# Performance work log

Measured on AMD Instinct MI355X. Metric: run time of the kernel, lower is better.

Reference implementation:

```python
import jax, jax.numpy as jnp
import numpy as np
from jax import lax


def _gru(x, h, Wi, Wh, bi, bh):
    # PyTorch GRUCell: gates ordered (r, z, n)
    gi = x @ Wi + bi
    gh = h @ Wh + bh
    ir, iz, in_ = jnp.split(gi, 3, axis=-1)
    hr, hz, hn = jnp.split(gh, 3, axis=-1)
    r = jax.nn.sigmoid(ir + hr)
    z = jax.nn.sigmoid(iz + hz)
    n = jnp.tanh(in_ + r * hn)
    return (1.0 - z) * n + z * h


def _mlp(x, W1, b1, W2, b2):
    return jax.nn.leaky_relu(x @ W1 + b1, 0.1) @ W2 + b2


def setup_inputs() -> dict:
    key = jax.random.key(0)
    S, Wn, E, DH, OD = 128, 3968, 128, 512, 2  # scenarios, world agents, embed, dec hidden, out dim
    N, H = S + Wn, 4 * E
    ks = jax.random.split(key, 32)
    rn = lambda k, sh, s: (jax.random.normal(k, sh, jnp.float32) * s)
    # ragged segment ids: every scenario gets >=1 world agent, rest random
    extra = jax.random.randint(ks[0], (Wn - S,), 0, S)
    seg_ids = jnp.sort(jnp.concatenate([jnp.arange(S), extra])).astype(jnp.int32)
    sH = 1.0 / np.sqrt(H)
    return {
        'goals': rn(ks[1], (N, 2), 1.0),
        'agn_dyn': rn(ks[2], (N, E), 1.0),
        'agn_ccls': rn(ks[3], (N, E), 1.0),
        'agn_int': rn(ks[4], (N, E), 1.0),
        'seg_ids': seg_ids,
        'sdc_h0': rn(ks[5], (S, H), 1.0),
        'wld_h0': rn(ks[6], (Wn, H), 1.0),
        'gol_W': rn(ks[7], (2, E), 1.0 / np.sqrt(2.0)),
        'gol_b': rn(ks[8], (E,), 0.01),
        'sdc_Wi': rn(ks[9], (H, 3 * H), sH), 'sdc_Wh': rn(ks[10], (H, 3 * H), sH),
        'sdc_bi': rn(ks[11], (3 * H,), 0.01), 'sdc_bh': rn(ks[12], (3 * H,), 0.01),
        'wld_Wi': rn(ks[13], (H, 3 * H), sH), 'wld_Wh': rn(ks[14], (H, 3 * H), sH),
        'wld_bi': rn(ks[15], (3 * H,), 0.01), 'wld_bh': rn(ks[16], (3 * H,), 0.01),
        'sdc_o1W': rn(ks[17], (H, DH), sH), 'sdc_o1b': rn(ks[18], (DH,), 0.01),
        'sdc_o2W': rn(ks[19], (DH, OD), 1.0 / np.sqrt(DH)), 'sdc_o2b': rn(ks[20], (OD,), 0.01),
        'wld_o1W': rn(ks[21], (H, DH), sH), 'wld_o1b': rn(ks[22], (DH,), 0.01),
        'wld_o2W': rn(ks[23], (DH, OD), 1.0 / np.sqrt(DH)), 'wld_o2b': rn(ks[24], (OD,), 0.01),
    }


def reference(goals, agn_dyn, agn_ccls, agn_int, seg_ids, sdc_h0, wld_h0,
              gol_W, gol_b, sdc_Wi, sdc_Wh, sdc_bi, sdc_bh,
              wld_Wi, wld_Wh, wld_bi, wld_bh,
              sdc_o1W, sdc_o1b, sdc_o2W, sdc_o2b,
              wld_o1W, wld_o1b, wld_o2W, wld_o2b):
    S = sdc_h0.shape[0]
    agn_gol = goals @ gol_W + gol_b                                  # [N, E]
    enc = jnp.concatenate([agn_gol, agn_dyn, agn_ccls, agn_int], 1)  # [N, 4E]
    sdc_h = _gru(enc[:S], sdc_h0, sdc_Wi, sdc_Wh, sdc_bi, sdc_bh)    # step 0
    wld_h = _gru(enc[S:], wld_h0, wld_Wi, wld_Wh, wld_bi, wld_bh)

    def step(carry, _):
        sh, wh = carry
        sdc_in = jax.ops.segment_max(wh, seg_ids, num_segments=S,
                                     indices_are_sorted=True)        # per-scenario max-pool
        wld_in = sh[seg_ids]                                         # broadcast SDC to its group
        sh2 = _gru(sdc_in, sh, sdc_Wi, sdc_Wh, sdc_bi, sdc_bh)
        wh2 = _gru(wld_in, wh, wld_Wi, wld_Wh, wld_bi, wld_bh)
        return (sh2, wh2), (sh2, wh2)

    (_, _), (sdc_hs, wld_hs) = lax.scan(step, (sdc_h, wld_h), None, length=79)
    sdc_all = jnp.concatenate([sdc_h[None], sdc_hs], 0).transpose(1, 0, 2)  # [S, 80, 4E]
    wld_all = jnp.concatenate([wld_h[None], wld_hs], 0).transpose(1, 0, 2)  # [W, 80, 4E]
    out_sdc = _mlp(sdc_all, sdc_o1W, sdc_o1b, sdc_o2W, sdc_o2b)
    out_wld = _mlp(wld_all, wld_o1W, wld_o1b, wld_o2W, wld_o2b)
    return jnp.concatenate([out_sdc, out_wld], 0)                    # [N, 80, out_dim]
```

## Files before the change

### kernel.cpp

```cpp
#include <hip/hip_runtime.h>


typedef __attribute__((ext_vector_type(8))) short short8;
typedef __attribute__((ext_vector_type(4))) float f32x4;
typedef unsigned short u16;
typedef unsigned int u32;

#define DEV __device__ __forceinline__

constexpr int S  = 128;
constexpr int NR = 4096;
constexpr int H  = 512;
constexpr int TH = 1536;
constexpr int SLOT = NR * H;
constexpr int SEGSZ = S * H;

struct P {
  const float *goals, *dyn, *ccls, *inte;
  const int *seg;
  const float *sdc_h0, *wld_h0;
  const float *golW, *golb;
  const float *sdcbi, *sdcbh, *wldbi, *wldbh;
  const float *sdco1b, *sdco2W, *sdco2b;
  const float *wldo1b, *wldo2W, *wldo2b;
  const float *sdcWi, *sdcWh, *wldWi, *wldWh, *sdco1W, *wldo1W;
  float *out;
  float *whf;
  u16   *ring;
  u16   *enc;
  u16   *WT;
  u16   *o1T;
  float *G;
  u32   *segb;
  u16   *segbf;
  float *part;
  int t;
};

DEV u16 f2bf(float f) {
  u32 u = __float_as_uint(f);
  u32 r = u + 0x7FFFu + ((u >> 16) & 1u);
  return (u16)(r >> 16);
}
DEV u32 flipf(float f) {
  u32 u = __float_as_uint(f);
  return (u & 0x80000000u) ? ~u : (u | 0x80000000u);
}
DEV float unflip(u32 s) {
  u32 u = (s & 0x80000000u) ? (s & 0x7FFFFFFFu) : ~s;
  return __uint_as_float(u);
}
DEV float sigm(float x)  { return 1.0f / (1.0f + __expf(-x)); }
DEV float tanh_(float x) { return 2.0f / (1.0f + __expf(-2.0f * x)) - 1.0f; }

DEV f32x4 mfma16(short8 a, short8 b, f32x4 c) {
  return __builtin_amdgcn_mfma_f32_16x16x32_bf16(a, b, c, 0, 0, 0);
}

DEV void gload16(const void* g, void* l) {
  __builtin_amdgcn_global_load_lds(
      (const __attribute__((address_space(1))) void*)g,
      (__attribute__((address_space(3))) void*)l, 16, 0, 0);
}

DEV short8 lds_frag(const u16* lds, int row, int g) {
  return *(const short8*)(lds + row * 64 + ((g ^ (row & 7)) << 3));
}

__global__ __launch_bounds__(256) void k_prep(P p) {
  const int b = blockIdx.x, tid = threadIdx.x;
  __shared__ float ltf[64 * 65];
  if (b < 896) {
    int nt, kt, Nn; const float* src; u16* dst;
    if (b < 768) {
      int m = b / 192, t2 = b % 192;
      nt = t2 % 24; kt = t2 / 24; Nn = TH;
      src = (m == 0) ? p.sdcWi : (m == 1) ? p.sdcWh : (m == 2) ? p.wldWi : p.wldWh;
      dst = p.WT + m * TH * H;
    } else {
      int bb = b - 768, m = bb / 64, t2 = bb % 64;
      nt = t2 % 8; kt = t2 / 8; Nn = H;
      src = m ? p.wldo1W : p.sdco1W;
      dst = p.o1T + m * H * H;
    }
    for (int it = 0; it < 16; ++it) {
      int kl = it * 4 + (tid >> 6), nl = tid & 63;
      ltf[nl * 65 + kl] = src[(kt * 64 + kl) * Nn + nt * 64 + nl];
    }
    __syncthreads();
    for (int it = 0; it < 2; ++it) {
      int nl = it * 32 + (tid >> 3), k8 = (tid & 7) * 8;
      short8 v;
#pragma unroll
      for (int e = 0; e < 8; ++e) v[e] = (short)f2bf(ltf[nl * 65 + k8 + e]);
      *(short8*)(dst + (nt * 64 + nl) * H + kt * 64 + k8) = v;
    }
  } else if (b < 960) {
    int r0 = (b - 896) * 64;
    for (int i = 0; i < 128; ++i) {
      int idx = i * 256 + tid, row = r0 + (idx >> 9), c = idx & 511;
      float v;
      if (c < 128)      v = p.goals[row*2]*p.golW[c] + p.goals[row*2+1]*p.golW[128+c] + p.golb[c];
      else if (c < 256) v = p.dyn [row*128 + c - 128];
      else if (c < 384) v = p.ccls[row*128 + c - 256];
      else              v = p.inte[row*128 + c - 384];
      p.enc[row * H + c] = f2bf(v);
    }
  } else if (b < 1024) {
    int r0 = (b - 960) * 64;
    for (int i = 0; i < 128; ++i) {
      int idx = i * 256 + tid, row = r0 + (idx >> 9), c = idx & 511;
      float v = (row < S) ? p.sdc_h0[row * H + c] : p.wld_h0[(row - S) * H + c];
      p.whf[SLOT + row * H + c] = v;
      p.ring[7 * SLOT + row * H + c] = f2bf(v);
    }
  } else {
    int base = (b - 1024) * 16384;
    for (int i = 0; i < 64; ++i) p.segb[base + i * 256 + tid] = 0u;
  }
}

__global__ __launch_bounds__(256) void k_big0(P p) {
  const int b = blockIdx.x, tid = threadIdx.x;
  const int rt = b >> 3, cg = b & 7;
  const bool sdc = rt < 2;
  const int w = tid >> 6, lr = (tid >> 4) & 3, lc = tid & 15;
  __shared__ u16 sm[16384];
  const u16* WiT = p.WT + (sdc ? 0 : 2) * TH * H;
  const u16* WhT = p.WT + (sdc ? 1 : 3) * TH * H;

  f32x4 ai[3][4], ah[3][4];
  f32x4 zero = {0.f, 0.f, 0.f, 0.f};
#pragma unroll
  for (int g = 0; g < 3; ++g)
#pragma unroll
    for (int mt = 0; mt < 4; ++mt) { ai[g][mt] = zero; ah[g][mt] = zero; }

  for (int pass = 0; pass < 2; ++pass) {
    const u16* A  = pass ? (p.ring + 7 * SLOT + rt * 64 * H) : (p.enc + rt * 64 * H);
    const u16* BT = pass ? WhT : WiT;
    for (int kc = 0; kc < H; kc += 64) {
      __syncthreads();
#pragma unroll
      for (int it = 0; it < 8; ++it) {
        int u = it * 256 + tid;
        int gs = (u ^ (u >> 3)) & 7;
        const u16* src;
        if (u < 512) {
          src = A + (u >> 3) * H + kc + gs * 8;
        } else {
          int v = u - 512;
          int g = v >> 9, m = (v >> 3) & 63;
          src = BT + (g * H + cg * 64 + m) * H + kc + gs * 8;
        }
        gload16(src, sm + (it * 256 + (tid & 192)) * 8);
      }
      __syncthreads();
#pragma unroll
      for (int s2 = 0; s2 < 2; ++s2) {
        const int gk = s2 * 4 + lr;
        short8 av[4], bv[3];
#pragma unroll
        for (int mt = 0; mt < 4; ++mt) av[mt] = lds_frag(sm, mt * 16 + lc, gk);
#pragma unroll
        for (int g = 0; g < 3; ++g) bv[g] = lds_frag(sm + 4096 + g * 4096, w * 16 + lc, gk);
#pragma unroll
        for (int g = 0; g < 3; ++g)
#pragma unroll
          for (int mt = 0; mt < 4; ++mt) {
            f32x4 r = pass ? ah[g][mt] : ai[g][mt];
            r = mfma16(av[mt], bv[g], r);
            if (pass) ah[g][mt] = r; else ai[g][mt] = r;
          }
      }
    }
  }
  const float* bi = sdc ? p.sdcbi : p.wldbi;
  const float* bh = sdc ? p.sdcbh : p.wldbh;
  const int col = cg * 64 + w * 16 + lc;
  const float bir = bi[col], biz = bi[H + col], bin = bi[2 * H + col];
  const float bhr = bh[col], bhz = bh[H + col], bhn = bh[2 * H + col];
#pragma unroll
  for (int mt = 0; mt < 4; ++mt)
#pragma unroll
    for (int i = 0; i < 4; ++i) {
      int grow = rt * 64 + mt * 16 + lr * 4 + i;
      float r = sigm(ai[0][mt][i] + bir + ah[0][mt][i] + bhr);
      float z = sigm(ai[1][mt][i] + biz + ah[1][mt][i] + bhz);
      float n = tanh_(ai[2][mt][i] + bin + r * (ah[2][mt][i] + bhn));
      float h = p.whf[SLOT + grow * H + col];
      float h2 = (1.f - z) * n + z * h;
      p.whf[grow * H + col] = h2;
      p.ring[grow * H + col] = f2bf(h2);
      if (!sdc) {
        int scen = p.seg[grow - S];
        atomicMax(p.segb + scen * H + col, flipf(h2));
      }
    }
}

__global__ __launch_bounds__(512) void k_small(P p) {
  const int b = blockIdx.x, tid = threadIdx.x;
  const int gtid = b * 512 + tid;
  u32* sb = p.segb + (p.t & 1) * SEGSZ;
  if (gtid < 16384) ((uint4*)sb)[gtid] = make_uint4(0u, 0u, 0u, 0u);
  const u32* sp = p.segb + ((p.t - 1) & 1) * SEGSZ;
  if (gtid < 16384) {
    uint4 q = ((const uint4*)sp)[gtid];
    u32 lo = (u32)f2bf(unflip(q.x)) | ((u32)f2bf(unflip(q.y)) << 16);
    u32 hi = (u32)f2bf(unflip(q.z)) | ((u32)f2bf(unflip(q.w)) << 16);
    ((u32*)p.segbf)[gtid * 2]     = lo;
    ((u32*)p.segbf)[gtid * 2 + 1] = hi;
  }
  const int rh = b / 24, nc = b % 24;
  const int wv = tid >> 6, wm = wv >> 2, wn = wv & 3;
  const int lr = (tid >> 4) & 3, lc = tid & 15;
  __shared__ u16 sm[16384];
  const u16* Ab = p.ring + ((p.t - 1) & 7) * SLOT + rh * 64 * H;
  const u16* Wb = p.WT + 2 * TH * H;

  f32x4 acc[2];
  f32x4 zero = {0.f, 0.f, 0.f, 0.f};
  acc[0] = zero; acc[1] = zero;

  for (int kc = 0; kc < H; kc += 128) {
    __syncthreads();
#pragma unroll
    for (int it = 0; it < 4; ++it) {
      int u = it * 512 + tid;
      int q = u >> 9;
      int m = (u >> 3) & 63, g = u & 7;
      int gs = g ^ (m & 7);
      int ko = kc + ((q & 1) << 6) + gs * 8;
      const u16* src = (q < 2) ? (Ab + m * H + ko)
                               : (Wb + (nc * 64 + m) * H + ko);
      gload16(src, sm + (it * 512 + (tid & 448)) * 8);
    }
    __syncthreads();
#pragma unroll
    for (int c = 0; c < 2; ++c)
#pragma unroll
      for (int s2 = 0; s2 < 2; ++s2) {
        const int gk = s2 * 4 + lr;
        short8 bv = lds_frag(sm + (2 + c) * 4096, wn * 16 + lc, gk);
#pragma unroll
        for (int mt = 0; mt < 2; ++mt)
          acc[mt] = mfma16(
              lds_frag(sm + c * 4096, wm * 32 + mt * 16 + lc, gk), bv, acc[mt]);
      }
  }
  const int colb = nc * 64 + wn * 16 + lc;
  const float bi = p.wldbi[colb];
#pragma unroll
  for (int mt = 0; mt < 2; ++mt)
#pragma unroll
    for (int i = 0; i < 4; ++i)
      p.G[(rh * 64 + wm * 32 + mt * 16 + lr * 4 + i) * TH + colb] = acc[mt][i] + bi;
}

__global__ __launch_bounds__(512) void k_big(P p) {
  const int b = blockIdx.x, tid = threadIdx.x;
  const int lr = (tid >> 4) & 3, lc = tid & 15;
  __shared__ u16 sm[16384];
  const int tp = (p.t - 1) & 7, tn = p.t & 7;
  const float* whfP = p.whf + ((p.t - 1) & 1) * SLOT;
  float* whfN = p.whf + (p.t & 1) * SLOT;
  u16* ringN = p.ring + tn * SLOT;

  if (b < 496) {
    const int wv = tid >> 6, wm = wv >> 2, wn = wv & 3;
    const int rt = b >> 3, cg = b & 7;
    const u16* Abase = p.ring + tp * SLOT + (S + rt * 64) * H;
    const u16* Bbase = p.WT + 3 * TH * H;
    f32x4 acc[3][2];
    f32x4 zero = {0.f, 0.f, 0.f, 0.f};
#pragma unroll
    for (int g = 0; g < 3; ++g) { acc[g][0] = zero; acc[g][1] = zero; }

    for (int kc = 0; kc < H; kc += 64) {
      __syncthreads();
#pragma unroll
      for (int it = 0; it < 4; ++it) {
        int u = it * 512 + tid;
        int gs = (u ^ (u >> 3)) & 7;
        const u16* src;
        if (u < 512) {
          src = Abase + (u >> 3) * H + kc + gs * 8;
        } else {
          int v = u - 512;
          int g = v >> 9, m = (v >> 3) & 63;
          src = Bbase + (g * H + cg * 64 + m) * H + kc + gs * 8;
        }
        gload16(src, sm + (it * 512 + (tid & 448)) * 8);
      }
      __syncthreads();
#pragma unroll
      for (int s2 = 0; s2 < 2; ++s2) {
        const int gk = s2 * 4 + lr;
        short8 av[2], bv[3];
#pragma unroll
        for (int mt = 0; mt < 2; ++mt)
          av[mt] = lds_frag(sm, wm * 32 + mt * 16 + lc, gk);
#pragma unroll
        for (int g = 0; g < 3; ++g)
          bv[g] = lds_frag(sm + 4096 + g * 4096, wn * 16 + lc, gk);
#pragma unroll
        for (int g = 0; g < 3; ++g)
#pragma unroll
          for (int mt = 0; mt < 2; ++mt) acc[g][mt] = mfma16(av[mt], bv[g], acc[g][mt]);
      }
    }
    const int col = cg * 64 + wn * 16 + lc;
    const float bhr = p.wldbh[col], bhz = p.wldbh[H + col], bhn = p.wldbh[2 * H + col];
    u32* sb = p.segb + (p.t & 1) * SEGSZ;
    int curSc = -1; float curMx = 0.f;
#pragma unroll
    for (int mt = 0; mt < 2; ++mt)
#pragma unroll
      for (int i = 0; i < 4; ++i) {
        int wrow = rt * 64 + wm * 32 + mt * 16 + lr * 4 + i;
        int grow = S + wrow;
        int scen = p.seg[wrow];
        const float* Gr = p.G + scen * TH;
        float r = sigm(Gr[col]          + acc[0][mt][i] + bhr);
        float z = sigm(Gr[H + col]      + acc[1][mt][i] + bhz);
        float n = tanh_(Gr[2 * H + col] + r * (acc[2][mt][i] + bhn));
        float h = whfP[grow * H + col];
        float h2 = (1.f - z) * n + z * h;
        whfN[grow * H + col] = h2;
        ringN[grow * H + col] = f2bf(h2);
        if (scen == curSc) curMx = fmaxf(curMx, h2);
        else {
          if (curSc >= 0) atomicMax(sb + curSc * H + col, flipf(curMx));
          curSc = scen; curMx = h2;
        }
      }
    atomicMax(sb + curSc * H + col, flipf(curMx));
  } else {
    const int w = tid >> 6;
    if (w >= 4) return;
    const int ab = b - 496, rh = ab >> 5, cgx = ab & 31;
    f32x4 ai[3], ah[3];
    f32x4 zero = {0.f, 0.f, 0.f, 0.f};
#pragma unroll
    for (int g = 0; g < 3; ++g) { ai[g] = zero; ah[g] = zero; }

    for (int pass = 0; pass < 2; ++pass) {
      const u16* A  = pass ? (p.ring + tp * SLOT + rh * 64 * H)
                           : (p.segbf + rh * 64 * H);
      const u16* BT = p.WT + (pass ? 1 : 0) * TH * H;
      for (int kc = 0; kc < H; kc += 64) {
        __syncthreads();
#pragma unroll
        for (int it = 0; it < 4; ++it) {
          int u = it * 256 + tid;
          if (u < 896) {
            int gs = (u ^ (u >> 3)) & 7;
            const u16* src;
            if (u < 512) {
              src = A + (u >> 3) * H + kc + gs * 8;
            } else {
              int v = u - 512;
              int m = v >> 3;
              src = BT + ((m >> 4) * H + cgx * 16 + (m & 15)) * H + kc + gs * 8;
            }
            gload16(src, sm + (it * 256 + (tid & 192)) * 8);
          }
        }
        __syncthreads();
#pragma unroll
        for (int s2 = 0; s2 < 2; ++s2) {
          const int gk = s2 * 4 + lr;
          short8 a = lds_frag(sm, w * 16 + lc, gk);
#pragma unroll
          for (int g = 0; g < 3; ++g) {
            f32x4 r = pass ? ah[g] : ai[g];
            r = mfma16(a, lds_frag(sm + 4096, g * 16 + lc, gk), r);
            if (pass) ah[g] = r; else ai[g] = r;
          }
        }
      }
    }
    const int col = cgx * 16 + lc;
    const float bir = p.sdcbi[col], biz = p.sdcbi[H + col], bin = p.sdcbi[2 * H + col];
    const float bhr = p.sdcbh[col], bhz = p.sdcbh[H + col], bhn = p.sdcbh[2 * H + col];
#pragma unroll
    for (int i = 0; i < 4; ++i) {
      int srow = rh * 64 + w * 16 + lr * 4 + i;
      float r = sigm(ai[0][i] + bir + ah[0][i] + bhr);
      float z = sigm(ai[1][i] + biz + ah[1][i] + bhz);
      float n = tanh_(ai[2][i] + bin + r * (ah[2][i] + bhn));
      float h = whfP[srow * H + col];
      float h2 = (1.f - z) * n + z * h;
      whfN[srow * H + col] = h2;
      ringN[srow * H + col] = f2bf(h2);
    }
  }
}

__global__ __launch_bounds__(256) void k_mlp(P p) {
  const int b = blockIdx.x, tid = threadIdx.x;
  const int rt = b >> 2, ct = b & 3;
  const int slot = rt >> 5, rtile = rt & 31;
  const bool sdc = (rtile == 0);
  const int w = tid >> 6, lr = (tid >> 4) & 3, lc = tid & 15;
  __shared__ u16 sm[16384];
  const u16* A  = p.ring + slot * SLOT + rtile * 128 * H;
  const u16* Bb = p.o1T + (sdc ? 0 : 1) * H * H + (ct * 128) * H;
  const float* o1b = sdc ? p.sdco1b : p.wldo1b;
  const float* o2W = sdc ? p.sdco2W : p.wldo2W;

  f32x4 acc[8][2];
  f32x4 zero = {0.f, 0.f, 0.f, 0.f};
#pragma unroll
  for (int mt = 0; mt < 8; ++mt) { acc[mt][0] = zero; acc[mt][1] = zero; }

  for (int kc = 0; kc < H; kc += 64) {
    __syncthreads();
#pragma unroll
    for (int it = 0; it < 8; ++it) {
      int u = it * 256 + tid;
      int gs = (u ^ (u >> 3)) & 7;
      const u16* src;
      if (u < 1024) src = A  + (u >> 3) * H + kc + gs * 8;
      else          src = Bb + ((u >> 3) & 127) * H + kc + gs * 8;
      gload16(src, sm + (it * 256 + (tid & 192)) * 8);
    }
    __syncthreads();
#pragma unroll
    for (int s2 = 0; s2 < 2; ++s2) {
      const int gk = s2 * 4 + lr;
      short8 av[8], bv[2];
#pragma unroll
      for (int mt = 0; mt < 8; ++mt) av[mt] = lds_frag(sm, mt * 16 + lc, gk);
#pragma unroll
      for (int c2 = 0; c2 < 2; ++c2) bv[c2] = lds_frag(sm + 8192, w * 32 + c2 * 16 + lc, gk);
#pragma unroll
      for (int mt = 0; mt < 8; ++mt)
#pragma unroll
        for (int c2 = 0; c2 < 2; ++c2) acc[mt][c2] = mfma16(av[mt], bv[c2], acc[mt][c2]);
    }
  }
  __syncthreads();
  float* red = (float*)sm;
#pragma unroll
  for (int mt = 0; mt < 8; ++mt) {
    float q0[4] = {0.f, 0.f, 0.f, 0.f}, q1[4] = {0.f, 0.f, 0.f, 0.f};
#pragma unroll
    for (int c2 = 0; c2 < 2; ++c2) {
      int col = ct * 128 + w * 32 + c2 * 16 + lc;
      float b1 = o1b[col], w0 = o2W[col * 2], w1 = o2W[col * 2 + 1];
#pragma unroll
      for (int i = 0; i < 4; ++i) {
        float v = acc[mt][c2][i] + b1;
        v = v > 0.f ? v : 0.1f * v;
        q0[i] += v * w0; q1[i] += v * w1;
      }
    }
#pragma unroll
    for (int off = 1; off < 16; off <<= 1)
#pragma unroll
      for (int i = 0; i < 4; ++i) {
        q0[i] += __shfl_xor(q0[i], off);
        q1[i] += __shfl_xor(q1[i], off);
      }
    if (lc == 0)
#pragma unroll
      for (int i = 0; i < 4; ++i) {
        int row = mt * 16 + lr * 4 + i;
        red[(w * 128 + row) * 2 + 0] = q0[i];
        red[(w * 128 + row) * 2 + 1] = q1[i];
      }
  }
  __syncthreads();
  {
    int row = tid >> 1, od = tid & 1;
    float sum = red[(0 * 128 + row) * 2 + od] + red[(1 * 128 + row) * 2 + od] +
                red[(2 * 128 + row) * 2 + od] + red[(3 * 128 + row) * 2 + od];
    int r = slot * 4096 + rtile * 128 + row;
    p.part[ct * 65536 + r * 2 + od] = sum;
  }
}

__global__ __launch_bounds__(256) void k_mlp2(P p) {
  const int gtid = blockIdx.x * 256 + threadIdx.x;
  for (int i = gtid; i < 65536; i += 16384) {
    int r = i >> 1, od = i & 1;
    int row = r & 4095, slot = r >> 12;
    float v = p.part[i] + p.part[65536 + i] + p.part[131072 + i] + p.part[196608 + i];
    v += (row < S ? p.sdco2b : p.wldo2b)[od];
    p.out[row * 160 + (p.t + slot) * 2 + od] = v;
  }
}

extern "C" void kernel_launch(void* const* d_in, const int* in_sizes, int n_in,
                              void* d_out, int out_size, void* d_ws, size_t ws_size,
                              hipStream_t stream) {
  P prm;
  prm.goals  = (const float*)d_in[0];
  prm.dyn    = (const float*)d_in[1];
  prm.ccls   = (const float*)d_in[2];
  prm.inte   = (const float*)d_in[3];
  prm.seg    = (const int*)  d_in[4];
  prm.sdc_h0 = (const float*)d_in[5];
  prm.wld_h0 = (const float*)d_in[6];
  prm.golW   = (const float*)d_in[7];
  prm.golb   = (const float*)d_in[8];
  prm.sdcWi  = (const float*)d_in[9];
  prm.sdcWh  = (const float*)d_in[10];
  prm.sdcbi  = (const float*)d_in[11];
  prm.sdcbh  = (const float*)d_in[12];
  prm.wldWi  = (const float*)d_in[13];
  prm.wldWh  = (const float*)d_in[14];
  prm.wldbi  = (const float*)d_in[15];
  prm.wldbh  = (const float*)d_in[16];
  prm.sdco1W = (const float*)d_in[17];
  prm.sdco1b = (const float*)d_in[18];
  prm.sdco2W = (const float*)d_in[19];
  prm.sdco2b = (const float*)d_in[20];
  prm.wldo1W = (const float*)d_in[21];
  prm.wldo1b = (const float*)d_in[22];
  prm.wldo2W = (const float*)d_in[23];
  prm.wldo2b = (const float*)d_in[24];
  prm.out = (float*)d_out;

  char* ws = (char*)d_ws;
  prm.whf   = (float*)(ws + 0);
  prm.ring  = (u16*)  (ws + 16777216);
  prm.enc   = (u16*)  (ws + 50331648);
  prm.WT    = (u16*)  (ws + 54525952);
  prm.o1T   = (u16*)  (ws + 60817408);
  prm.G     = (float*)(ws + 61865984);
  prm.segb  = (u32*)  (ws + 62652416);
  prm.segbf = (u16*)  (ws + 50331648);
  prm.part  = (float*)(ws + 50331648 + 131072);

  prm.t = 0;
  k_prep<<<1028, 256, 0, stream>>>(prm);
  k_big0<<<512, 256, 0, stream>>>(prm);
  for (int t = 1; t < 80; ++t) {
    prm.t = t;
    k_small<<<48, 512, 0, stream>>>(prm);
    k_big<<<560, 512, 0, stream>>>(prm);
    if ((t & 7) == 7) {
      P pm = prm;
      pm.t = t - 7;
      k_mlp<<<1024, 256, 0, stream>>>(pm);
      k_mlp2<<<64, 256, 0, stream>>>(pm);
    }
  }
}
```

Measured before the change: 2.442 ms.

## Move SDC GRU step into small kernel and fuse MLP reduction into step

```diff
diff --git a/kernel.cpp b/kernel.cpp
--- a/kernel.cpp
+++ b/kernel.cpp
@@ -32,7 +32,6 @@
   u16   *o1T;
   float *G;
   u32   *segb;
-  u16   *segbf;
   float *part;
   int t;
 };
@@ -63,6 +62,22 @@
       (__attribute__((address_space(3))) void*)l, 16, 0, 0);
 }
 
+DEV void stage_bf(u16* lds, const u16* src, int stride, int rows, int tid) {
+  for (int u = tid; u < rows * 8; u += 256) {
+    int m = u >> 3, g = u & 7, gs = g ^ (m & 7);
+    *(short8*)(lds + (u << 3)) = *(const short8*)(src + m * stride + (gs << 3));
+  }
+}
+DEV void stage_seg(u16* lds, const u32* src, int stride, int tid) {
+  for (int u = tid; u < 512; u += 256) {
+    int m = u >> 3, g = u & 7, gs = g ^ (m & 7);
+    const u32* pp = src + m * stride + (gs << 3);
+    short8 v;
+#pragma unroll
+    for (int e = 0; e < 8; ++e) v[e] = (short)f2bf(unflip(pp[e]));
+    *(short8*)(lds + (u << 3)) = v;
+  }
+}
 DEV short8 lds_frag(const u16* lds, int row, int g) {
   return *(const short8*)(lds + row * 64 + ((g ^ (row & 7)) << 3));
 }
@@ -97,22 +112,34 @@
     }
   } else if (b < 960) {
     int r0 = (b - 896) * 64;
-    for (int i = 0; i < 128; ++i) {
-      int idx = i * 256 + tid, row = r0 + (idx >> 9), c = idx & 511;
-      float v;
-      if (c < 128)      v = p.goals[row*2]*p.golW[c] + p.goals[row*2+1]*p.golW[128+c] + p.golb[c];
-      else if (c < 256) v = p.dyn [row*128 + c - 128];
-      else if (c < 384) v = p.ccls[row*128 + c - 256];
-      else              v = p.inte[row*128 + c - 384];
-      p.enc[row * H + c] = f2bf(v);
+    for (int i = 0; i < 32; ++i) {
+      int idx = i * 256 + tid;
+      int row = r0 + (idx >> 7), c4 = (idx & 127) * 4;
+      float4 v;
+      if (c4 < 128) {
+        float g0 = p.goals[row * 2], g1 = p.goals[row * 2 + 1];
+        v.x = g0 * p.golW[c4]     + g1 * p.golW[128 + c4]     + p.golb[c4];
+        v.y = g0 * p.golW[c4 + 1] + g1 * p.golW[128 + c4 + 1] + p.golb[c4 + 1];
+        v.z = g0 * p.golW[c4 + 2] + g1 * p.golW[128 + c4 + 2] + p.golb[c4 + 2];
+        v.w = g0 * p.golW[c4 + 3] + g1 * p.golW[128 + c4 + 3] + p.golb[c4 + 3];
+      } else if (c4 < 256) v = *(const float4*)(p.dyn  + row * 128 + c4 - 128);
+      else if (c4 < 384)   v = *(const float4*)(p.ccls + row * 128 + c4 - 256);
+      else                 v = *(const float4*)(p.inte + row * 128 + c4 - 384);
+      ushort4 o;
+      o.x = f2bf(v.x); o.y = f2bf(v.y); o.z = f2bf(v.z); o.w = f2bf(v.w);
+      *(ushort4*)(p.enc + row * H + c4) = o;
     }
   } else if (b < 1024) {
     int r0 = (b - 960) * 64;
-    for (int i = 0; i < 128; ++i) {
-      int idx = i * 256 + tid, row = r0 + (idx >> 9), c = idx & 511;
-      float v = (row < S) ? p.sdc_h0[row * H + c] : p.wld_h0[(row - S) * H + c];
-      p.whf[SLOT + row * H + c] = v;
-      p.ring[7 * SLOT + row * H + c] = f2bf(v);
+    for (int i = 0; i < 32; ++i) {
+      int idx = i * 256 + tid;
+      int row = r0 + (idx >> 7), c4 = (idx & 127) * 4;
+      float4 v = (row < S) ? *(const float4*)(p.sdc_h0 + row * H + c4)
+                           : *(const float4*)(p.wld_h0 + (row - S) * H + c4);
+      *(float4*)(p.whf + SLOT + row * H + c4) = v;
+      ushort4 o;
+      o.x = f2bf(v.x); o.y = f2bf(v.y); o.z = f2bf(v.z); o.w = f2bf(v.w);
+      *(ushort4*)(p.ring + 7 * SLOT + row * H + c4) = o;
     }
   } else {
     int base = (b - 1024) * 16384;
@@ -120,21 +147,22 @@
   }
 }
 
-__global__ __launch_bounds__(256) void k_big0(P p) {
+__global__ __launch_bounds__(512) void k_big0(P p) {
   const int b = blockIdx.x, tid = threadIdx.x;
   const int rt = b >> 3, cg = b & 7;
   const bool sdc = rt < 2;
-  const int w = tid >> 6, lr = (tid >> 4) & 3, lc = tid & 15;
+  const int wv = tid >> 6, wm = wv >> 2, wn = wv & 3;
+  const int lr = (tid >> 4) & 3, lc = tid & 15;
   __shared__ u16 sm[16384];
   const u16* WiT = p.WT + (sdc ? 0 : 2) * TH * H;
   const u16* WhT = p.WT + (sdc ? 1 : 3) * TH * H;
 
-  f32x4 ai[3][4], ah[3][4];
+  f32x4 ai[3][2], ah[3][2];
   f32x4 zero = {0.f, 0.f, 0.f, 0.f};
 #pragma unroll
   for (int g = 0; g < 3; ++g)
 #pragma unroll
-    for (int mt = 0; mt < 4; ++mt) { ai[g][mt] = zero; ah[g][mt] = zero; }
+    for (int mt = 0; mt < 2; ++mt) { ai[g][mt] = zero; ah[g][mt] = zero; }
 
   for (int pass = 0; pass < 2; ++pass) {
     const u16* A  = pass ? (p.ring + 7 * SLOT + rt * 64 * H) : (p.enc + rt * 64 * H);
@@ -142,8 +170,8 @@
     for (int kc = 0; kc < H; kc += 64) {
       __syncthreads();
 #pragma unroll
-      for (int it = 0; it < 8; ++it) {
-        int u = it * 256 + tid;
+      for (int it = 0; it < 4; ++it) {
+        int u = it * 512 + tid;
         int gs = (u ^ (u >> 3)) & 7;
         const u16* src;
         if (u < 512) {
@@ -153,21 +181,23 @@
           int g = v >> 9, m = (v >> 3) & 63;
           src = BT + (g * H + cg * 64 + m) * H + kc + gs * 8;
         }
-        gload16(src, sm + (it * 256 + (tid & 192)) * 8);
+        gload16(src, sm + (it * 512 + (tid & 448)) * 8);
       }
       __syncthreads();
 #pragma unroll
       for (int s2 = 0; s2 < 2; ++s2) {
         const int gk = s2 * 4 + lr;
-        short8 av[4], bv[3];
-#pragma unroll
-        for (int mt = 0; mt < 4; ++mt) av[mt] = lds_frag(sm, mt * 16 + lc, gk);
-#pragma unroll
-        for (int g = 0; g < 3; ++g) bv[g] = lds_frag(sm + 4096 + g * 4096, w * 16 + lc, gk);
+        short8 av[2], bv[3];
+#pragma unroll
+        for (int mt = 0; mt < 2; ++mt)
+          av[mt] = lds_frag(sm, wm * 32 + mt * 16 + lc, gk);
 #pragma unroll
         for (int g = 0; g < 3; ++g)
-#pragma unroll
-          for (int mt = 0; mt < 4; ++mt) {
+          bv[g] = lds_frag(sm + 4096 + g * 4096, wn * 16 + lc, gk);
+#pragma unroll
+        for (int g = 0; g < 3; ++g)
+#pragma unroll
+          for (int mt = 0; mt < 2; ++mt) {
             f32x4 r = pass ? ah[g][mt] : ai[g][mt];
             r = mfma16(av[mt], bv[g], r);
             if (pass) ah[g][mt] = r; else ai[g][mt] = r;
@@ -177,14 +207,14 @@
   }
   const float* bi = sdc ? p.sdcbi : p.wldbi;
   const float* bh = sdc ? p.sdcbh : p.wldbh;
-  const int col = cg * 64 + w * 16 + lc;
+  const int col = cg * 64 + wn * 16 + lc;
   const float bir = bi[col], biz = bi[H + col], bin = bi[2 * H + col];
   const float bhr = bh[col], bhz = bh[H + col], bhn = bh[2 * H + col];
 #pragma unroll
-  for (int mt = 0; mt < 4; ++mt)
+  for (int mt = 0; mt < 2; ++mt)
 #pragma unroll
     for (int i = 0; i < 4; ++i) {
-      int grow = rt * 64 + mt * 16 + lr * 4 + i;
+      int grow = rt * 64 + wm * 32 + mt * 16 + lr * 4 + i;
       float r = sigm(ai[0][mt][i] + bir + ah[0][mt][i] + bhr);
       float z = sigm(ai[1][mt][i] + biz + ah[1][mt][i] + bhz);
       float n = tanh_(ai[2][mt][i] + bin + r * (ah[2][mt][i] + bhn));
@@ -201,181 +231,94 @@
 
 __global__ __launch_bounds__(512) void k_small(P p) {
   const int b = blockIdx.x, tid = threadIdx.x;
-  const int gtid = b * 512 + tid;
-  u32* sb = p.segb + (p.t & 1) * SEGSZ;
-  if (gtid < 16384) ((uint4*)sb)[gtid] = make_uint4(0u, 0u, 0u, 0u);
-  const u32* sp = p.segb + ((p.t - 1) & 1) * SEGSZ;
-  if (gtid < 16384) {
-    uint4 q = ((const uint4*)sp)[gtid];
-    u32 lo = (u32)f2bf(unflip(q.x)) | ((u32)f2bf(unflip(q.y)) << 16);
-    u32 hi = (u32)f2bf(unflip(q.z)) | ((u32)f2bf(unflip(q.w)) << 16);
-    ((u32*)p.segbf)[gtid * 2]     = lo;
-    ((u32*)p.segbf)[gtid * 2 + 1] = hi;
-  }
-  const int rh = b / 24, nc = b % 24;
-  const int wv = tid >> 6, wm = wv >> 2, wn = wv & 3;
-  const int lr = (tid >> 4) & 3, lc = tid & 15;
-  __shared__ u16 sm[16384];
-  const u16* Ab = p.ring + ((p.t - 1) & 7) * SLOT + rh * 64 * H;
-  const u16* Wb = p.WT + 2 * TH * H;
-
-  f32x4 acc[2];
-  f32x4 zero = {0.f, 0.f, 0.f, 0.f};
-  acc[0] = zero; acc[1] = zero;
-
-  for (int kc = 0; kc < H; kc += 128) {
-    __syncthreads();
-#pragma unroll
-    for (int it = 0; it < 4; ++it) {
-      int u = it * 512 + tid;
-      int q = u >> 9;
-      int m = (u >> 3) & 63, g = u & 7;
-      int gs = g ^ (m & 7);
-      int ko = kc + ((q & 1) << 6) + gs * 8;
-      const u16* src = (q < 2) ? (Ab + m * H + ko)
-                               : (Wb + (nc * 64 + m) * H + ko);
-      gload16(src, sm + (it * 512 + (tid & 448)) * 8);
-    }
-    __syncthreads();
-#pragma unroll
-    for (int c = 0; c < 2; ++c)
-#pragma unroll
-      for (int s2 = 0; s2 < 2; ++s2) {
-        const int gk = s2 * 4 + lr;
-        short8 bv = lds_frag(sm + (2 + c) * 4096, wn * 16 + lc, gk);
-#pragma unroll
-        for (int mt = 0; mt < 2; ++mt)
-          acc[mt] = mfma16(
-              lds_frag(sm + c * 4096, wm * 32 + mt * 16 + lc, gk), bv, acc[mt]);
-      }
-  }
-  const int colb = nc * 64 + wn * 16 + lc;
-  const float bi = p.wldbi[colb];
-#pragma unroll
-  for (int mt = 0; mt < 2; ++mt)
-#pragma unroll
-    for (int i = 0; i < 4; ++i)
-      p.G[(rh * 64 + wm * 32 + mt * 16 + lr * 4 + i) * TH + colb] = acc[mt][i] + bi;
-}
-
-__global__ __launch_bounds__(512) void k_big(P p) {
-  const int b = blockIdx.x, tid = threadIdx.x;
-  const int lr = (tid >> 4) & 3, lc = tid & 15;
   __shared__ u16 sm[16384];
   const int tp = (p.t - 1) & 7, tn = p.t & 7;
-  const float* whfP = p.whf + ((p.t - 1) & 1) * SLOT;
-  float* whfN = p.whf + (p.t & 1) * SLOT;
-  u16* ringN = p.ring + tn * SLOT;
-
-  if (b < 496) {
+
+  if (b < 48) {
+    const int gtid = b * 512 + tid;
+    u32* sb = p.segb + (p.t & 1) * SEGSZ;
+    if (gtid < 16384) ((uint4*)sb)[gtid] = make_uint4(0u, 0u, 0u, 0u);
+
+    const int rh = b / 24, nc = b % 24;
     const int wv = tid >> 6, wm = wv >> 2, wn = wv & 3;
-    const int rt = b >> 3, cg = b & 7;
-    const u16* Abase = p.ring + tp * SLOT + (S + rt * 64) * H;
-    const u16* Bbase = p.WT + 3 * TH * H;
-    f32x4 acc[3][2];
+    const int lr = (tid >> 4) & 3, lc = tid & 15;
+    const u16* Ab = p.ring + tp * SLOT + rh * 64 * H;
+    const u16* Wb = p.WT + 2 * TH * H;
+
+    f32x4 acc[2];
     f32x4 zero = {0.f, 0.f, 0.f, 0.f};
-#pragma unroll
-    for (int g = 0; g < 3; ++g) { acc[g][0] = zero; acc[g][1] = zero; }
-
-    for (int kc = 0; kc < H; kc += 64) {
+    acc[0] = zero; acc[1] = zero;
+
+    for (int kc = 0; kc < H; kc += 128) {
       __syncthreads();
 #pragma unroll
       for (int it = 0; it < 4; ++it) {
         int u = it * 512 + tid;
-        int gs = (u ^ (u >> 3)) & 7;
-        const u16* src;
-        if (u < 512) {
-          src = Abase + (u >> 3) * H + kc + gs * 8;
-        } else {
-          int v = u - 512;
-          int g = v >> 9, m = (v >> 3) & 63;
-          src = Bbase + (g * H + cg * 64 + m) * H + kc + gs * 8;
+        int q = u >> 9;
+        int m = (u >> 3) & 63, g = u & 7;
+        int gs = g ^ (m & 7);
+        int ko = kc + ((q & 1) << 6) + gs * 8;
+        const u16* src = (q < 2) ? (Ab + m * H + ko)
+                                 : (Wb + (nc * 64 + m) * H + ko);
+        gload16(src, sm + (it * 512 + (tid & 448)) * 8);
+      }
+      __syncthreads();
+#pragma unroll
+      for (int c = 0; c < 2; ++c)
+#pragma unroll
+        for (int s2 = 0; s2 < 2; ++s2) {
+          const int gk = s2 * 4 + lr;
+          short8 bv = lds_frag(sm + (2 + c) * 4096, wn * 16 + lc, gk);
+#pragma unroll
+          for (int mt = 0; mt < 2; ++mt)
+            acc[mt] = mfma16(
+                lds_frag(sm + c * 4096, wm * 32 + mt * 16 + lc, gk), bv, acc[mt]);
         }
-        gload16(src, sm + (it * 512 + (tid & 448)) * 8);
-      }
-      __syncthreads();
-#pragma unroll
-      for (int s2 = 0; s2 < 2; ++s2) {
-        const int gk = s2 * 4 + lr;
-        short8 av[2], bv[3];
-#pragma unroll
-        for (int mt = 0; mt < 2; ++mt)
-          av[mt] = lds_frag(sm, wm * 32 + mt * 16 + lc, gk);
-#pragma unroll
-        for (int g = 0; g < 3; ++g)
-          bv[g] = lds_frag(sm + 4096 + g * 4096, wn * 16 + lc, gk);
-#pragma unroll
-        for (int g = 0; g < 3; ++g)
-#pragma unroll
-          for (int mt = 0; mt < 2; ++mt) acc[g][mt] = mfma16(av[mt], bv[g], acc[g][mt]);
-      }
-    }
-    const int col = cg * 64 + wn * 16 + lc;
-    const float bhr = p.wldbh[col], bhz = p.wldbh[H + col], bhn = p.wldbh[2 * H + col];
-    u32* sb = p.segb + (p.t & 1) * SEGSZ;
-    int curSc = -1; float curMx = 0.f;
+    }
+    const int colb = nc * 64 + wn * 16 + lc;
+    const float bi = p.wldbi[colb];
 #pragma unroll
     for (int mt = 0; mt < 2; ++mt)
 #pragma unroll
-      for (int i = 0; i < 4; ++i) {
-        int wrow = rt * 64 + wm * 32 + mt * 16 + lr * 4 + i;
-        int grow = S + wrow;
-        int scen = p.seg[wrow];
-        const float* Gr = p.G + scen * TH;
-        float r = sigm(Gr[col]          + acc[0][mt][i] + bhr);
-        float z = sigm(Gr[H + col]      + acc[1][mt][i] + bhz);
-        float n = tanh_(Gr[2 * H + col] + r * (acc[2][mt][i] + bhn));
-        float h = whfP[grow * H + col];
-        float h2 = (1.f - z) * n + z * h;
-        whfN[grow * H + col] = h2;
-        ringN[grow * H + col] = f2bf(h2);
-        if (scen == curSc) curMx = fmaxf(curMx, h2);
-        else {
-          if (curSc >= 0) atomicMax(sb + curSc * H + col, flipf(curMx));
-          curSc = scen; curMx = h2;
-        }
-      }
-    atomicMax(sb + curSc * H + col, flipf(curMx));
-  } else {
+      for (int i = 0; i < 4; ++i)
+        p.G[(rh * 64 + wm * 32 + mt * 16 + lr * 4 + i) * TH + colb] = acc[mt][i] + bi;
+  } else if (b < 112) {
     const int w = tid >> 6;
     if (w >= 4) return;
-    const int ab = b - 496, rh = ab >> 5, cgx = ab & 31;
+    const int ab = b - 48, rh = ab >> 5, cgx = ab & 31;
+    const int lr = (tid >> 4) & 3, lc = tid & 15;
+    const u16* WiT = p.WT;
+    const u16* WhT = p.WT + 1 * TH * H;
+    u16* ldsA = sm;
+    u16* ldsB = sm + 4096;
+    const float* whfP = p.whf + ((p.t - 1) & 1) * SLOT;
+    float* whfN = p.whf + (p.t & 1) * SLOT;
+    u16* ringN = p.ring + tn * SLOT;
     f32x4 ai[3], ah[3];
     f32x4 zero = {0.f, 0.f, 0.f, 0.f};
 #pragma unroll
     for (int g = 0; g < 3; ++g) { ai[g] = zero; ah[g] = zero; }
 
+    const u32* segP = p.segb + ((p.t - 1) & 1) * SEGSZ;
     for (int pass = 0; pass < 2; ++pass) {
-      const u16* A  = pass ? (p.ring + tp * SLOT + rh * 64 * H)
-                           : (p.segbf + rh * 64 * H);
-      const u16* BT = p.WT + (pass ? 1 : 0) * TH * H;
+      const u16* Ab = p.ring + tp * SLOT + rh * 64 * H;
+      const u16* BT = pass ? WhT : WiT;
       for (int kc = 0; kc < H; kc += 64) {
         __syncthreads();
-#pragma unroll
-        for (int it = 0; it < 4; ++it) {
-          int u = it * 256 + tid;
-          if (u < 896) {
-            int gs = (u ^ (u >> 3)) & 7;
-            const u16* src;
-            if (u < 512) {
-              src = A + (u >> 3) * H + kc + gs * 8;
-            } else {
-              int v = u - 512;
-              int m = v >> 3;
-              src = BT + ((m >> 4) * H + cgx * 16 + (m & 15)) * H + kc + gs * 8;
-            }
-            gload16(src, sm + (it * 256 + (tid & 192)) * 8);
-          }
-        }
+        if (pass) stage_bf(ldsA, Ab + kc, H, 64, tid);
+        else      stage_seg(ldsA, segP + rh * 64 * H + kc, H, tid);
+#pragma unroll
+        for (int g = 0; g < 3; ++g)
+          stage_bf(ldsB + g * 1024, BT + (g * H + cgx * 16) * H + kc, H, 16, tid);
         __syncthreads();
 #pragma unroll
         for (int s2 = 0; s2 < 2; ++s2) {
           const int gk = s2 * 4 + lr;
-          short8 a = lds_frag(sm, w * 16 + lc, gk);
+          short8 a = lds_frag(ldsA, w * 16 + lc, gk);
 #pragma unroll
           for (int g = 0; g < 3; ++g) {
             f32x4 r = pass ? ah[g] : ai[g];
-            r = mfma16(a, lds_frag(sm + 4096, g * 16 + lc, gk), r);
+            r = mfma16(a, lds_frag(ldsB + g * 1024, lc, gk), r);
             if (pass) ah[g] = r; else ai[g] = r;
           }
         }
@@ -395,7 +338,97 @@
       whfN[srow * H + col] = h2;
       ringN[srow * H + col] = f2bf(h2);
     }
-  }
+  } else {
+    if ((p.t & 7) != 0 || p.t < 8) return;
+    const int base = p.t - 8;
+    const int gt2 = (b - 112) * 512 + tid;
+    for (int i = gt2; i < 65536; i += 32768) {
+      int r = i >> 1, od = i & 1;
+      int row = r & 4095, slot = r >> 12;
+      float v = p.part[i] + p.part[65536 + i] + p.part[131072 + i] + p.part[196608 + i];
+      v += (row < S ? p.sdco2b : p.wldo2b)[od];
+      p.out[row * 160 + (base + slot) * 2 + od] = v;
+    }
+  }
+}
+
+__global__ __launch_bounds__(512) void k_big(P p) {
+  const int b = blockIdx.x, tid = threadIdx.x;
+  const int lr = (tid >> 4) & 3, lc = tid & 15;
+  __shared__ u16 sm[16384];
+  const int tp = (p.t - 1) & 7, tn = p.t & 7;
+  const float* whfP = p.whf + ((p.t - 1) & 1) * SLOT;
+  float* whfN = p.whf + (p.t & 1) * SLOT;
+  u16* ringN = p.ring + tn * SLOT;
+
+  const int wv = tid >> 6, wm = wv >> 2, wn = wv & 3;
+  const int rt = b >> 3, cg = b & 7;
+  const u16* Abase = p.ring + tp * SLOT + (S + rt * 64) * H;
+  const u16* Bbase = p.WT + 3 * TH * H;
+  f32x4 acc[3][2];
+  f32x4 zero = {0.f, 0.f, 0.f, 0.f};
+#pragma unroll
+  for (int g = 0; g < 3; ++g) { acc[g][0] = zero; acc[g][1] = zero; }
+
+  for (int kc = 0; kc < H; kc += 64) {
+    __syncthreads();
+#pragma unroll
+    for (int it = 0; it < 4; ++it) {
+      int u = it * 512 + tid;
+      int gs = (u ^ (u >> 3)) & 7;
+      const u16* src;
+      if (u < 512) {
+        src = Abase + (u >> 3) * H + kc + gs * 8;
+      } else {
+        int v = u - 512;
+        int g = v >> 9, m = (v >> 3) & 63;
+        src = Bbase + (g * H + cg * 64 + m) * H + kc + gs * 8;
+      }
+      gload16(src, sm + (it * 512 + (tid & 448)) * 8);
+    }
+    __syncthreads();
+#pragma unroll
+    for (int s2 = 0; s2 < 2; ++s2) {
+      const int gk = s2 * 4 + lr;
+      short8 av[2], bv[3];
+#pragma unroll
+      for (int mt = 0; mt < 2; ++mt)
+        av[mt] = lds_frag(sm, wm * 32 + mt * 16 + lc, gk);
+#pragma unroll
+      for (int g = 0; g < 3; ++g)
+        bv[g] = lds_frag(sm + 4096 + g * 4096, wn * 16 + lc, gk);
+#pragma unroll
+      for (int g = 0; g < 3; ++g)
+#pragma unroll
+        for (int mt = 0; mt < 2; ++mt) acc[g][mt] = mfma16(av[mt], bv[g], acc[g][mt]);
+    }
+  }
+  const int col = cg * 64 + wn * 16 + lc;
+  const float bhr = p.wldbh[col], bhz = p.wldbh[H + col], bhn = p.wldbh[2 * H + col];
+  u32* sb = p.segb + (p.t & 1) * SEGSZ;
+  int curSc = -1; float curMx = 0.f;
+#pragma unroll
+  for (int mt = 0; mt < 2; ++mt)
+#pragma unroll
+    for (int i = 0; i < 4; ++i) {
+      int wrow = rt * 64 + wm * 32 + mt * 16 + lr * 4 + i;
+      int grow = S + wrow;
+      int scen = p.seg[wrow];
+      const float* Gr = p.G + scen * TH;
+      float r = sigm(Gr[col]          + acc[0][mt][i] + bhr);
+      float z = sigm(Gr[H + col]      + acc[1][mt][i] + bhz);
+      float n = tanh_(Gr[2 * H + col] + r * (acc[2][mt][i] + bhn));
+      float h = whfP[grow * H + col];
+      float h2 = (1.f - z) * n + z * h;
+      whfN[grow * H + col] = h2;
+      ringN[grow * H + col] = f2bf(h2);
+      if (scen == curSc) curMx = fmaxf(curMx, h2);
+      else {
+        if (curSc >= 0) atomicMax(sb + curSc * H + col, flipf(curMx));
+        curSc = scen; curMx = h2;
+      }
+    }
+  atomicMax(sb + curSc * H + col, flipf(curMx));
 }
 
 __global__ __launch_bounds__(256) void k_mlp(P p) {
@@ -532,21 +565,20 @@
   prm.o1T   = (u16*)  (ws + 60817408);
   prm.G     = (float*)(ws + 61865984);
   prm.segb  = (u32*)  (ws + 62652416);
-  prm.segbf = (u16*)  (ws + 50331648);
   prm.part  = (float*)(ws + 50331648 + 131072);
 
   prm.t = 0;
   k_prep<<<1028, 256, 0, stream>>>(prm);
-  k_big0<<<512, 256, 0, stream>>>(prm);
+  k_big0<<<512, 512, 0, stream>>>(prm);
   for (int t = 1; t < 80; ++t) {
     prm.t = t;
-    k_small<<<48, 512, 0, stream>>>(prm);
-    k_big<<<560, 512, 0, stream>>>(prm);
+    k_small<<<176, 512, 0, stream>>>(prm);
+    k_big<<<496, 512, 0, stream>>>(prm);
     if ((t & 7) == 7) {
-      P pm = prm;
-      pm.t = t - 7;
-      k_mlp<<<1024, 256, 0, stream>>>(pm);
-      k_mlp2<<<64, 256, 0, stream>>>(pm);
-    }
-  }
-}
+      k_mlp<<<1024, 256, 0, stream>>>(prm);
+    }
+  }
+  P pm = prm;
+  pm.t = 72;
+  k_mlp2<<<64, 256, 0, stream>>>(pm);
+}
```

New measurement: 3.675 ms. +50.5%, slower.
